# Kernel tuning notes

Measured on AMD Instinct MI355X. Metric: run time of the kernel, lower is better.

The kernel has to match this reference:

```python
import jax, jax.numpy as jnp
import numpy as np

B, H, LQ, LK, D, HID = 2, 1, 512, 512, 64, 128


def setup_inputs() -> dict:
    key = jax.random.key(0)
    ks = jax.random.split(key, 8)
    f = lambda k, shape, s=1.0: jax.random.normal(k, shape, dtype=jnp.float32) * s
    return {
        "q": f(ks[0], (B, H, LQ, D)),
        "k": f(ks[1], (B, H, LK, D)),
        "v": f(ks[2], (B, H, LK, D)),
        "mask": jnp.zeros((B, H, LQ, LK), jnp.float32),
        # shared q/k/v projection (self.w) and output projection (self.dense)
        "Ww": f(ks[3], (D, D), 0.1), "wb": jnp.zeros((D,), jnp.float32),
        "Wd": f(ks[4], (D, D), 0.1), "db": jnp.zeros((D,), jnp.float32),
        # two-layer MLP NN: 2*D -> HID -> 1
        "W1": f(ks[5], (2 * D, HID), 0.1), "b1": jnp.zeros((HID,), jnp.float32),
        "W2": f(ks[6], (HID, 1), 0.1), "b2": jnp.zeros((1,), jnp.float32),
    }


def _sim_scores(q, k, W1, b1, W2, b2, make_sym):
    # Equivalent to tile+concat+MLP, but splits W1 so the 2*D concat tensor
    # is never materialized; only the [B,H,Lq,Lk,HID] hidden is.
    W1q, W1k = W1[:D], W1[D:]
    qa = q @ W1q  # [B,H,Lq,HID]
    kb = k @ W1k  # [B,H,Lk,HID]
    h = jax.nn.relu(qa[:, :, :, None, :] + kb[:, :, None, :, :] + b1)
    s = (h @ W2)[..., 0] + b2[0]  # [B,H,Lq,Lk]
    if make_sym:
        # concat([k, q]) order: hidden2 = relu(k_j @ W1q + q_i @ W1k + b1)
        qb = q @ W1k
        ka = k @ W1q
        h2 = jax.nn.relu(qb[:, :, :, None, :] + ka[:, :, None, :, :] + b1)
        s = s + (h2 @ W2)[..., 0] + b2[0]
    return s


def reference(q, k, v, mask, Ww, wb, Wd, db, W1, b1, W2, b2):
    make_sym = True
    qp = q @ Ww + wb
    kp = k @ Ww + wb
    vp = v @ Ww + wb
    logits = _sim_scores(qp, kp, W1, b1, W2, b2, make_sym)
    logits = logits + mask * (-1e9)
    attn = jax.nn.softmax(logits, axis=-1)  # [B,H,Lq,Lk]
    out = attn @ vp                          # [B,H,Lq,D]
    out = out @ Wd + db
    return (out, attn)
```

## Files before the change

### kernel.cpp

```cpp
#include <hip/hip_runtime.h>
#include <hip/hip_bf16.h>


#define NROWS 1024
#define DD    64
#define HH    128
#define LK_   512
#define QR    4

__global__ __launch_bounds__(128)
void proj_kernel(const float* __restrict__ q, const float* __restrict__ k,
                 const float* __restrict__ v,
                 const float* __restrict__ Ww, const float* __restrict__ wb,
                 const float* __restrict__ W1, const float* __restrict__ b1,
                 float* __restrict__ vp,
                 float* __restrict__ qa, float* __restrict__ qb,
                 float* __restrict__ kaTf, float* __restrict__ kbTf)
{
    const int r    = blockIdx.x;
    const int type = r >> 10;
    const int idx  = r & 1023;
    const int t    = threadIdx.x;

    const float* src = (type == 0) ? q : (type == 1) ? k : v;

    __shared__ float x[DD];
    __shared__ float xp[DD];

    if (t < DD) x[t] = src[idx * DD + t];
    __syncthreads();

    if (t < DD) {
        float acc = wb[t];
        #pragma unroll
        for (int c = 0; c < DD; ++c) acc = fmaf(x[c], Ww[c * DD + t], acc);
        xp[t] = acc;
        if (type == 2) vp[idx * DD + t] = acc;
    }
    __syncthreads();

    if (type == 2) return;

    float accA = 0.f;
    float accB = 0.f;
    #pragma unroll
    for (int d = 0; d < DD; ++d) {
        const float xv = xp[d];
        accA = fmaf(xv, W1[d * HH + t],        accA);
        accB = fmaf(xv, W1[(DD + d) * HH + t], accB);
    }
    if (type == 0) {
        qa[idx * HH + t] = accA + b1[t];
        qb[idx * HH + t] = accB + b1[t];
    } else {
        const int b  = idx >> 9;
        const int j  = idx & (LK_ - 1);
        const int o  = ((b * (HH / 4) + (t >> 2)) * LK_ + j) * 4 + (t & 3);
        kaTf[o] = accA;
        kbTf[o] = accB;
    }
}

__global__ __launch_bounds__(512)
void attn_kernel(const float* __restrict__ mask,
                 const float* __restrict__ vp,
                 const float* __restrict__ qa, const float* __restrict__ qb,
                 const float4* __restrict__ kaT, const float4* __restrict__ kbT,
                 const float* __restrict__ W2, const float* __restrict__ b2,
                 const float* __restrict__ Wd, const float* __restrict__ db,
                 float* __restrict__ out, float* __restrict__ attn)
{
    const int row0 = blockIdx.x * QR;
    const int b    = row0 >> 9;
    const int t    = threadIdx.x;
    const int wid  = t >> 6;
    const int lane = t & 63;
    const int j    = t;

    __shared__ float p_int[LK_ * QR];
    __shared__ float redm[8][QR];
    __shared__ float reds[8][QR];
    __shared__ float opart[8][QR][DD];
    __shared__ float o_l[QR][DD];

    const float4* kaTb = kaT + b * (HH / 4) * LK_;
    const float4* kbTb = kbT + b * (HH / 4) * LK_;
    const float*  qaR  = qa + row0 * HH;
    const float*  qbR  = qb + row0 * HH;
    const float4* w24  = reinterpret_cast<const float4*>(W2);

    float mk[QR];
    #pragma unroll
    for (int r = 0; r < QR; ++r) mk[r] = mask[(row0 + r) * LK_ + j];

    float s1[QR] = {0.f, 0.f, 0.f, 0.f};
    float s2[QR] = {0.f, 0.f, 0.f, 0.f};
    #pragma unroll 2
    for (int h4 = 0; h4 < HH / 4; ++h4) {
        const float4 w   = w24[h4];
        const float4 kb4 = kbTb[h4 * LK_ + j];
        const float4 ka4 = kaTb[h4 * LK_ + j];
        const int h = h4 * 4;
        #pragma unroll
        for (int r = 0; r < QR; ++r) {
            s1[r] = fmaf(fmaxf(qaR[r * HH + h + 0] + kb4.x, 0.f), w.x, s1[r]);
            s1[r] = fmaf(fmaxf(qaR[r * HH + h + 1] + kb4.y, 0.f), w.y, s1[r]);
            s1[r] = fmaf(fmaxf(qaR[r * HH + h + 2] + kb4.z, 0.f), w.z, s1[r]);
            s1[r] = fmaf(fmaxf(qaR[r * HH + h + 3] + kb4.w, 0.f), w.w, s1[r]);
            s2[r] = fmaf(fmaxf(qbR[r * HH + h + 0] + ka4.x, 0.f), w.x, s2[r]);
            s2[r] = fmaf(fmaxf(qbR[r * HH + h + 1] + ka4.y, 0.f), w.y, s2[r]);
            s2[r] = fmaf(fmaxf(qbR[r * HH + h + 2] + ka4.z, 0.f), w.z, s2[r]);
            s2[r] = fmaf(fmaxf(qbR[r * HH + h + 3] + ka4.w, 0.f), w.w, s2[r]);
        }
    }

    const float b2v = b2[0];
    float sv[QR];
    #pragma unroll
    for (int r = 0; r < QR; ++r)
        sv[r] = s1[r] + s2[r] + 2.f * b2v + mk[r] * (-1e9f);

    float m[QR];
    #pragma unroll
    for (int r = 0; r < QR; ++r) {
        float mv = sv[r];
        #pragma unroll
        for (int off = 32; off > 0; off >>= 1) mv = fmaxf(mv, __shfl_xor(mv, off));
        if (lane == 0) redm[wid][r] = mv;
    }
    __syncthreads();
    #pragma unroll
    for (int r = 0; r < QR; ++r) {
        float mv = redm[0][r];
        #pragma unroll
        for (int w = 1; w < 8; ++w) mv = fmaxf(mv, redm[w][r]);
        m[r] = mv;
    }

    float e[QR];
    #pragma unroll
    for (int r = 0; r < QR; ++r) {
        e[r] = expf(sv[r] - m[r]);
        float s = e[r];
        #pragma unroll
        for (int off = 32; off > 0; off >>= 1) s += __shfl_xor(s, off);
        if (lane == 0) reds[wid][r] = s;
    }
    __syncthreads();

    float pv[QR];
    #pragma unroll
    for (int r = 0; r < QR; ++r) {
        float s = reds[0][r];
        #pragma unroll
        for (int w = 1; w < 8; ++w) s += reds[w][r];
        pv[r] = e[r] / s;
        attn[(row0 + r) * LK_ + j] = pv[r];
    }
    *reinterpret_cast<float4*>(&p_int[j * QR]) =
        make_float4(pv[0], pv[1], pv[2], pv[3]);
    __syncthreads();

    float acc[QR] = {0.f, 0.f, 0.f, 0.f};
    {
        const int jb = wid * 64;
        const float* vpb = vp + (b * LK_ + jb) * DD;
        #pragma unroll 8
        for (int jj = 0; jj < 64; ++jj) {
            const float4 pj = *reinterpret_cast<const float4*>(&p_int[(jb + jj) * QR]);
            const float vv = vpb[jj * DD + lane];
            acc[0] = fmaf(pj.x, vv, acc[0]);
            acc[1] = fmaf(pj.y, vv, acc[1]);
            acc[2] = fmaf(pj.z, vv, acc[2]);
            acc[3] = fmaf(pj.w, vv, acc[3]);
        }
    }
    #pragma unroll
    for (int r = 0; r < QR; ++r) opart[wid][r][lane] = acc[r];
    __syncthreads();

    if (t < QR * DD) {
        const int r = t >> 6, d = t & 63;
        float o = opart[0][r][d];
        #pragma unroll
        for (int w = 1; w < 8; ++w) o += opart[w][r][d];
        o_l[r][d] = o;
    }
    __syncthreads();

    if (t < QR * DD) {
        const int r = t >> 6, d = t & 63;
        float res = db[d];
        #pragma unroll
        for (int c = 0; c < DD; ++c) res = fmaf(o_l[r][c], Wd[c * DD + d], res);
        out[(row0 + r) * DD + d] = res;
    }
}

extern "C" void kernel_launch(void* const* d_in, const int* in_sizes, int n_in,
                              void* d_out, int out_size, void* d_ws, size_t ws_size,
                              hipStream_t stream)
{
    const float* q    = (const float*)d_in[0];
    const float* k    = (const float*)d_in[1];
    const float* v    = (const float*)d_in[2];
    const float* mask = (const float*)d_in[3];
    const float* Ww   = (const float*)d_in[4];
    const float* wb   = (const float*)d_in[5];
    const float* Wd   = (const float*)d_in[6];
    const float* db   = (const float*)d_in[7];
    const float* W1   = (const float*)d_in[8];
    const float* b1   = (const float*)d_in[9];
    const float* W2   = (const float*)d_in[10];
    const float* b2   = (const float*)d_in[11];

    float* ws = (float*)d_ws;
    float* vp = ws;
    float* qa = vp + NROWS * DD;
    float* qb = qa + NROWS * HH;
    float* kaTf = qb + NROWS * HH;
    float* kbTf = kaTf + NROWS * HH;

    float* out  = (float*)d_out;
    float* attn = out + NROWS * DD;

    proj_kernel<<<dim3(3072), dim3(128), 0, stream>>>(
        q, k, v, Ww, wb, W1, b1, vp, qa, qb, kaTf, kbTf);

    attn_kernel<<<dim3(NROWS / QR), dim3(512), 0, stream>>>(
        mask, vp, qa, qb, (const float4*)kaTf, (const float4*)kbTf,
        W2, b2, Wd, db, out, attn);
}
```

Baseline: 102.0 us.

## Fold output projection into V and broadcast probabilities via readlane

Uses associativity to precompute (v@Ww+wb)@Wd in the projection kernel, so the attention kernel only adds the bias after P·V and the per-row 64x64 output GEMV plus its shared buffer and barrier go away. P·V now reads probabilities directly from registers with readlane instead of staging them in LDS, which drops the p_int shared array and one syncthreads. The rounding of the result changes slightly, and the fully unrolled 64-step readlane loop raises code size.

```diff
diff --git a/kernel.cpp b/kernel.cpp
--- a/kernel.cpp
+++ b/kernel.cpp
@@ -13,7 +13,8 @@
                  const float* __restrict__ v,
                  const float* __restrict__ Ww, const float* __restrict__ wb,
                  const float* __restrict__ W1, const float* __restrict__ b1,
-                 float* __restrict__ vp,
+                 const float* __restrict__ Wd,
+                 float* __restrict__ vpd,
                  float* __restrict__ qa, float* __restrict__ qb,
                  float* __restrict__ kaTf, float* __restrict__ kbTf)
 {
@@ -35,11 +36,18 @@
         #pragma unroll
         for (int c = 0; c < DD; ++c) acc = fmaf(x[c], Ww[c * DD + t], acc);
         xp[t] = acc;
-        if (type == 2) vp[idx * DD + t] = acc;
-    }
-    __syncthreads();
-
-    if (type == 2) return;
+    }
+    __syncthreads();
+
+    if (type == 2) {
+        if (t < DD) {
+            float acc = 0.f;
+            #pragma unroll
+            for (int c = 0; c < DD; ++c) acc = fmaf(xp[c], Wd[c * DD + t], acc);
+            vpd[idx * DD + t] = acc;
+        }
+        return;
+    }
 
     float accA = 0.f;
     float accB = 0.f;
@@ -63,11 +71,11 @@
 
 __global__ __launch_bounds__(512)
 void attn_kernel(const float* __restrict__ mask,
-                 const float* __restrict__ vp,
+                 const float* __restrict__ vpd,
                  const float* __restrict__ qa, const float* __restrict__ qb,
                  const float4* __restrict__ kaT, const float4* __restrict__ kbT,
                  const float* __restrict__ W2, const float* __restrict__ b2,
-                 const float* __restrict__ Wd, const float* __restrict__ db,
+                 const float* __restrict__ db,
                  float* __restrict__ out, float* __restrict__ attn)
 {
     const int row0 = blockIdx.x * QR;
@@ -77,11 +85,9 @@
     const int lane = t & 63;
     const int j    = t;
 
-    __shared__ float p_int[LK_ * QR];
     __shared__ float redm[8][QR];
     __shared__ float reds[8][QR];
     __shared__ float opart[8][QR][DD];
-    __shared__ float o_l[QR][DD];
 
     const float4* kaTb = kaT + b * (HH / 4) * LK_;
     const float4* kbTb = kbT + b * (HH / 4) * LK_;
@@ -157,22 +163,20 @@
         pv[r] = e[r] / s;
         attn[(row0 + r) * LK_ + j] = pv[r];
     }
-    *reinterpret_cast<float4*>(&p_int[j * QR]) =
-        make_float4(pv[0], pv[1], pv[2], pv[3]);
-    __syncthreads();
 
     float acc[QR] = {0.f, 0.f, 0.f, 0.f};
     {
         const int jb = wid * 64;
-        const float* vpb = vp + (b * LK_ + jb) * DD;
-        #pragma unroll 8
+        const float* vb = vpd + (b * LK_ + jb) * DD;
+        #pragma unroll
         for (int jj = 0; jj < 64; ++jj) {
-            const float4 pj = *reinterpret_cast<const float4*>(&p_int[(jb + jj) * QR]);
-            const float vv = vpb[jj * DD + lane];
-            acc[0] = fmaf(pj.x, vv, acc[0]);
-            acc[1] = fmaf(pj.y, vv, acc[1]);
-            acc[2] = fmaf(pj.z, vv, acc[2]);
-            acc[3] = fmaf(pj.w, vv, acc[3]);
+            const float vv = vb[jj * DD + lane];
+            #pragma unroll
+            for (int r = 0; r < QR; ++r) {
+                const float pj = __int_as_float(
+                    __builtin_amdgcn_readlane(__float_as_int(pv[r]), jj));
+                acc[r] = fmaf(pj, vv, acc[r]);
+            }
         }
     }
     #pragma unroll
@@ -184,16 +188,7 @@
         float o = opart[0][r][d];
         #pragma unroll
         for (int w = 1; w < 8; ++w) o += opart[w][r][d];
-        o_l[r][d] = o;
-    }
-    __syncthreads();
-
-    if (t < QR * DD) {
-        const int r = t >> 6, d = t & 63;
-        float res = db[d];
-        #pragma unroll
-        for (int c = 0; c < DD; ++c) res = fmaf(o_l[r][c], Wd[c * DD + d], res);
-        out[(row0 + r) * DD + d] = res;
+        out[(row0 + r) * DD + d] = o + db[d];
     }
 }
 
@@ -215,9 +210,9 @@
     const float* b2   = (const float*)d_in[11];
 
     float* ws = (float*)d_ws;
-    float* vp = ws;
-    float* qa = vp + NROWS * DD;
-    float* qb = qa + NROWS * HH;
+    float* vpd = ws;
+    float* qa  = vpd + NROWS * DD;
+    float* qb  = qa + NROWS * HH;
     float* kaTf = qb + NROWS * HH;
     float* kbTf = kaTf + NROWS * HH;
 
@@ -225,9 +220,9 @@
     float* attn = out + NROWS * DD;
 
     proj_kernel<<<dim3(3072), dim3(128), 0, stream>>>(
-        q, k, v, Ww, wb, W1, b1, vp, qa, qb, kaTf, kbTf);
+        q, k, v, Ww, wb, W1, b1, Wd, vpd, qa, qb, kaTf, kbTf);
 
     attn_kernel<<<dim3(NROWS / QR), dim3(512), 0, stream>>>(
-        mask, vp, qa, qb, (const float4*)kaTf, (const float4*)kbTf,
-        W2, b2, Wd, db, out, attn);
+        mask, vpd, qa, qb, (const float4*)kaTf, (const float4*)kbTf,
+        W2, b2, db, out, attn);
 }
```

Result: no change. 103.1 us (+1.0%).
